# Optimization experiments

Hardware: AMD Instinct MI355X
Metric: run time of the kernel (lower is better)

The kernel has to match this reference:

```python
import jax, jax.numpy as jnp
import numpy as np

N, IN, H, D, OUT = 2048, 256, 12, 32, 384
ALPHA = 0.2


def setup_inputs() -> dict:
    key = jax.random.key(0)
    ks = jax.random.split(key, 12)
    s = 0.05
    return {
        "x": jax.random.normal(ks[0], (N, IN), jnp.float32),
        "adj": jax.random.uniform(ks[1], (N, N), jnp.float32),  # all > 0 -> fully connected mask
        "W": jax.random.normal(ks[2], (H * D, IN), jnp.float32) * s,
        "attn_src": jax.random.normal(ks[3], (H, D), jnp.float32) * s,
        "attn_dst": jax.random.normal(ks[4], (H, D), jnp.float32) * s,
        "edge_W": jax.random.normal(ks[5], (H, 1), jnp.float32) * s,
        "edge_b": jax.random.normal(ks[6], (H,), jnp.float32) * s,
        "res_W": jax.random.normal(ks[7], (H * D, IN), jnp.float32) * s,
        "res_b": jax.random.normal(ks[8], (H * D,), jnp.float32) * s,
        "fus_W": jax.random.normal(ks[9], (OUT, H * D), jnp.float32) * s,
        "fus_b": jax.random.normal(ks[10], (OUT,), jnp.float32) * s,
    }


def reference(x, adj, W, attn_src, attn_dst, edge_W, edge_b, res_W, res_b, fus_W, fus_b):
    n = x.shape[0]
    h = (x @ W.T).reshape(n, H, D)                      # [N,H,D]
    a_src = jnp.einsum("nhd,hd->nh", h, attn_src)       # [N,H]
    a_dst = jnp.einsum("nhd,hd->nh", h, attn_dst)       # [N,H]
    attn = a_src[:, None, :] + a_dst[None, :, :]        # [N,N,H]
    # edge_encoder: Linear(1 -> H) applied to adj[...,None]
    attn = attn + adj[..., None] * edge_W.reshape(1, 1, H) + edge_b
    mask = (adj > 0)[..., None]                         # [N,N,1]
    attn = jnp.where(mask, attn, -jnp.inf)
    attn = jnp.where(attn >= 0, attn, ALPHA * attn)     # leaky_relu
    attn = jax.nn.softmax(attn, axis=1)                 # over source nodes j
    # dropout is identity in eval mode
    h_out = jnp.einsum("ijh,jhd->ihd", attn, h).reshape(n, H * D)
    h_out = h_out + x @ res_W.T + res_b                 # residual
    out = jax.nn.gelu(h_out @ fus_W.T + fus_b, approximate=False)
    return out
```

## Files before the change

kernel.cpp:

```cpp
#include <hip/hip_runtime.h>
#include <hip/hip_bf16.h>

#define NN 2048
#define NH 12
#define HD 32
#define CALL 384

typedef float f32x16 __attribute__((ext_vector_type(16)));
typedef _Float16 f16x4 __attribute__((ext_vector_type(4)));
typedef __fp16 fp16x2 __attribute__((ext_vector_type(2)));

static __device__ __forceinline__ f32x16 mfma8f16(f16x4 a, f16x4 b, f32x16 c) {
    return __builtin_amdgcn_mfma_f32_32x32x8f16(a, b, c, 0, 0, 0);
}
static __device__ __forceinline__ f16x4 u2f(uint2 u) {
    union { uint2 u2; f16x4 f; } c; c.u2 = u; return c.f;
}
static __device__ __forceinline__ void gload16(const void* gp, void* lp) {
    __builtin_amdgcn_global_load_lds(
        (const __attribute__((address_space(1))) unsigned int*)gp,
        (__attribute__((address_space(3))) unsigned int*)lp, 16, 0, 0);
}

__global__ __launch_bounds__(512) void gemm01(
    const float* __restrict__ A, const float* __restrict__ B0,
    const float* __restrict__ B1, const float* __restrict__ bias1,
    const float* __restrict__ attn_src, const float* __restrict__ attn_dst,
    _Float16* __restrict__ outT, float* __restrict__ outF,
    float* __restrict__ asrc, float* __restrict__ adstT)
{
    __shared__ __align__(16) char smem[17408];
    _Float16 (*As)[68] = (_Float16(*)[68])(smem);
    _Float16 (*Bs)[68] = (_Float16(*)[68])(smem + 8704);
    float* red = (float*)smem;

    const int t = threadIdx.x;
    const int w = t >> 6, l = t & 63, g = l >> 5, il = l & 31;
    const int q = w & 3, kg = w >> 2;
    const int m0 = blockIdx.x * 64, n0 = blockIdx.y * 64;
    const int mode = blockIdx.z;
    const float* B = mode ? B1 : B0;
    const int wr = (q >> 1) * 32, wc = (q & 1) * 32;
    const int ti = t >> 3, seg = t & 7;
    const int Kdim = 256;

    const float* Abase = A + (size_t)(m0 + ti) * Kdim + seg * 8;
    const float* Bbase = B + (size_t)(n0 + ti) * Kdim + seg * 8;

    f32x16 acc;
#pragma unroll
    for (int r = 0; r < 16; ++r) acc[r] = 0.f;

    float4 av0 = *reinterpret_cast<const float4*>(Abase);
    float4 av1 = *reinterpret_cast<const float4*>(Abase + 4);
    float4 bv0 = *reinterpret_cast<const float4*>(Bbase);
    float4 bv1 = *reinterpret_cast<const float4*>(Bbase + 4);

#pragma unroll 1
    for (int ss = 0; ss < 4; ++ss) {
        __syncthreads();
        {
            f16x4 lo = {(_Float16)av0.x, (_Float16)av0.y, (_Float16)av0.z, (_Float16)av0.w};
            f16x4 hi = {(_Float16)av1.x, (_Float16)av1.y, (_Float16)av1.z, (_Float16)av1.w};
            *reinterpret_cast<f16x4*>(&As[ti][seg * 8])     = lo;
            *reinterpret_cast<f16x4*>(&As[ti][seg * 8 + 4]) = hi;
            f16x4 lo2 = {(_Float16)bv0.x, (_Float16)bv0.y, (_Float16)bv0.z, (_Float16)bv0.w};
            f16x4 hi2 = {(_Float16)bv1.x, (_Float16)bv1.y, (_Float16)bv1.z, (_Float16)bv1.w};
            *reinterpret_cast<f16x4*>(&Bs[ti][seg * 8])     = lo2;
            *reinterpret_cast<f16x4*>(&Bs[ti][seg * 8 + 4]) = hi2;
        }
        __syncthreads();
        if (ss < 3) {
            const int kk = (ss + 1) * 64;
            av0 = *reinterpret_cast<const float4*>(Abase + kk);
            av1 = *reinterpret_cast<const float4*>(Abase + kk + 4);
            bv0 = *reinterpret_cast<const float4*>(Bbase + kk);
            bv1 = *reinterpret_cast<const float4*>(Bbase + kk + 4);
        }
#pragma unroll
        for (int kc = 0; kc < 4; ++kc) {
            f16x4 af = *reinterpret_cast<const f16x4*>(&As[wr + il][kg * 32 + kc * 8 + 4 * g]);
            f16x4 bf = *reinterpret_cast<const f16x4*>(&Bs[wc + il][kg * 32 + kc * 8 + 4 * g]);
            acc = mfma8f16(af, bf, acc);
        }
    }

    __syncthreads();
    if (kg == 1) {
#pragma unroll
        for (int r = 0; r < 16; ++r) red[(q * 16 + r) * 64 + l] = acc[r];
    }
    __syncthreads();
    if (kg != 0) return;
#pragma unroll
    for (int r = 0; r < 16; ++r) acc[r] += red[(q * 16 + r) * 64 + l];

    const int colg = n0 + wc + il;
    if (mode == 0) {
#pragma unroll
        for (int p = 0; p < 4; ++p) {
            const int row = m0 + wr + 8 * p + 4 * g;
            f16x4 v;
#pragma unroll
            for (int r = 0; r < 4; ++r) v[r] = (_Float16)acc[4 * p + r];
            *reinterpret_cast<f16x4*>(&outT[(size_t)colg * NN + row]) = v;
        }
        const int hstar = colg >> 5;
        const float sv = attn_src[hstar * HD + il];
        const float dv = attn_dst[hstar * HD + il];
        float ps[16], pd[16];
#pragma unroll
        for (int r = 0; r < 16; ++r) { ps[r] = acc[r] * sv; pd[r] = acc[r] * dv; }
#pragma unroll
        for (int m = 1; m <= 16; m <<= 1) {
#pragma unroll
            for (int r = 0; r < 16; ++r) {
                ps[r] += __shfl_xor(ps[r], m);
                pd[r] += __shfl_xor(pd[r], m);
            }
        }
        if (il == 0) {
#pragma unroll
            for (int r = 0; r < 16; ++r) {
                const int row = m0 + wr + (r & 3) + 8 * (r >> 2) + 4 * g;
                asrc[row * NH + hstar] = ps[r];
                adstT[(size_t)hstar * NN + row] = pd[r] * 1.44269504089f;
            }
        }
    } else {
        const float bs = bias1[colg];
#pragma unroll
        for (int r = 0; r < 16; ++r) {
            const int row = m0 + wr + (r & 3) + 8 * (r >> 2) + 4 * g;
            outF[(size_t)row * CALL + colg] = acc[r] + bs;
        }
    }
}

__global__ __launch_bounds__(512) void gemm2(
    const _Float16* __restrict__ A16, const float* __restrict__ B,
    const float* __restrict__ bias, float* __restrict__ outF)
{
    __shared__ __align__(16) char smem[17408];
    _Float16 (*As)[68] = (_Float16(*)[68])(smem);
    _Float16 (*Bs)[68] = (_Float16(*)[68])(smem + 8704);
    float* red = (float*)smem;

    const int t = threadIdx.x;
    const int w = t >> 6, l = t & 63, g = l >> 5, il = l & 31;
    const int q = w & 3, kg = w >> 2;
    const int m0 = blockIdx.x * 64, n0 = blockIdx.y * 64;
    const int wr = (q >> 1) * 32, wc = (q & 1) * 32;
    const int ti = t >> 3, seg = t & 7;
    const int Kdim = 384;

    const _Float16* Abase = A16 + (size_t)(m0 + ti) * Kdim + seg * 8;
    const float*    Bbase = B   + (size_t)(n0 + ti) * Kdim + seg * 8;

    f32x16 acc;
#pragma unroll
    for (int r = 0; r < 16; ++r) acc[r] = 0.f;

    uint4  av = *reinterpret_cast<const uint4*>(Abase);
    float4 bv0 = *reinterpret_cast<const float4*>(Bbase);
    float4 bv1 = *reinterpret_cast<const float4*>(Bbase + 4);

#pragma unroll 1
    for (int ss = 0; ss < 6; ++ss) {
        __syncthreads();
        {
            *reinterpret_cast<uint2*>(&As[ti][seg * 8])     = make_uint2(av.x, av.y);
            *reinterpret_cast<uint2*>(&As[ti][seg * 8 + 4]) = make_uint2(av.z, av.w);
            f16x4 lo = {(_Float16)bv0.x, (_Float16)bv0.y, (_Float16)bv0.z, (_Float16)bv0.w};
            f16x4 hi = {(_Float16)bv1.x, (_Float16)bv1.y, (_Float16)bv1.z, (_Float16)bv1.w};
            *reinterpret_cast<f16x4*>(&Bs[ti][seg * 8])     = lo;
            *reinterpret_cast<f16x4*>(&Bs[ti][seg * 8 + 4]) = hi;
        }
        __syncthreads();
        if (ss < 5) {
            const int kk = (ss + 1) * 64;
            av  = *reinterpret_cast<const uint4*>(Abase + kk);
            bv0 = *reinterpret_cast<const float4*>(Bbase + kk);
            bv1 = *reinterpret_cast<const float4*>(Bbase + kk + 4);
        }
#pragma unroll
        for (int kc = 0; kc < 4; ++kc) {
            f16x4 af = *reinterpret_cast<const f16x4*>(&As[wr + il][kg * 32 + kc * 8 + 4 * g]);
            f16x4 bf = *reinterpret_cast<const f16x4*>(&Bs[wc + il][kg * 32 + kc * 8 + 4 * g]);
            acc = mfma8f16(af, bf, acc);
        }
    }

    __syncthreads();
    if (kg == 1) {
#pragma unroll
        for (int r = 0; r < 16; ++r) red[(q * 16 + r) * 64 + l] = acc[r];
    }
    __syncthreads();
    if (kg != 0) return;
#pragma unroll
    for (int r = 0; r < 16; ++r) acc[r] += red[(q * 16 + r) * 64 + l];

    const int colg = n0 + wc + il;
    const float bs = bias[colg];
#pragma unroll
    for (int r = 0; r < 16; ++r) {
        const int row = m0 + wr + (r & 3) + 8 * (r >> 2) + 4 * g;
        float vv = acc[r] + bs;
        vv = 0.5f * vv * (1.0f + erff(vv * 0.70710678118f));
        outF[(size_t)row * CALL + colg] = vv;
    }
}

__global__ __launch_bounds__(1024, 4) void attn17(
    const float* __restrict__ adj, const _Float16* __restrict__ hT,
    const float* __restrict__ asrc, const float* __restrict__ adstT,
    const float* __restrict__ eW, const float* __restrict__ eb,
    const float* __restrict__ res, _Float16* __restrict__ hsum)
{
    __shared__ __align__(16) char smem[90112];
    const int t = threadIdx.x;
    const int w = t >> 6, l = t & 63, g = l >> 5, il = l & 31;
    const int band = blockIdx.x & 63, hg = blockIdx.x >> 6;
    const int i0 = band * 32, h0 = hg * 3, c0 = hg * 96;

    char* slice   = smem + w * 5632;
    char* adjb    = slice;
    float* adst_s = (float*)(slice + 4096);
    float* red    = (float*)smem;
    float* dsum_s = (float*)(smem + 49152);

    const float LOG2E = 1.44269504089f;
    const int jbase = w * 128;
    const float* abase = adj + (size_t)(i0 + il) * NN + jbase + 16 * g;

#pragma unroll
    for (int p = 0; p < 4; ++p)
        gload16(abase + 4 * p, adjb + p * 1024);

    float base_h[3], eWr[3];
#pragma unroll
    for (int hh = 0; hh < 3; ++hh) {
        base_h[hh] = (asrc[(size_t)(i0 + il) * NH + h0 + hh] + eb[h0 + hh]) * LOG2E;
        eWr[hh] = eW[h0 + hh] * LOG2E;
    }
#pragma unroll
    for (int p = 0; p < 6; ++p) {
        const int idx = p * 64 + l;
        adst_s[idx] = adstT[(size_t)(h0 + (idx >> 7)) * NN + jbase + (idx & 127)];
    }

    f32x16 acc[3];
#pragma unroll
    for (int hh = 0; hh < 3; ++hh)
#pragma unroll
        for (int r = 0; r < 16; ++r) acc[hh][r] = 0.f;
    float4 dsumv[3];
#pragma unroll
    for (int hh = 0; hh < 3; ++hh) dsumv[hh] = make_float4(0.f, 0.f, 0.f, 0.f);

    const _Float16* hbase = hT + (size_t)(c0 + il) * NN + jbase + 16 * g;

#pragma unroll 1
    for (int tl = 0; tl < 4; ++tl) {
        const int jo = tl * 32;
        asm volatile("s_waitcnt vmcnt(0)" ::: "memory");
        const float4 aj0 = *reinterpret_cast<const float4*>(adjb + 0 * 1024 + l * 16);
        const float4 aj1 = *reinterpret_cast<const float4*>(adjb + 1 * 1024 + l * 16);
        const float4 aj2 = *reinterpret_cast<const float4*>(adjb + 2 * 1024 + l * 16);
        const float4 aj3 = *reinterpret_cast<const float4*>(adjb + 3 * 1024 + l * 16);
        asm volatile("s_waitcnt lgkmcnt(0)" ::: "memory");
        if (tl < 3) {
#pragma unroll
            for (int p = 0; p < 4; ++p)
                gload16(abase + jo + 32 + 4 * p, adjb + p * 1024);
        }
        __builtin_amdgcn_s_setprio(1);
#pragma unroll
        for (int hh = 0; hh < 3; ++hh) {
            const _Float16* hp = hbase + (size_t)(hh * 32) * NN + jo;
            const uint4 hA = *reinterpret_cast<const uint4*>(hp);
            const uint4 hB = *reinterpret_cast<const uint4*>(hp + 8);
#pragma unroll
            for (int ks = 0; ks < 4; ++ks) {
                const float4 a4 = (ks == 0) ? aj0 : (ks == 1) ? aj1 : (ks == 2) ? aj2 : aj3;
                const float4 ad = *reinterpret_cast<const float4*>(
                    &adst_s[hh * 128 + jo + 16 * g + 4 * ks]);
                float e0, e1, e2, e3;
#pragma unroll
                for (int jj = 0; jj < 4; ++jj) {
                    const float ajv = (&a4.x)[jj];
                    float tt = fmaf(ajv, eWr[hh], base_h[hh] + (&ad.x)[jj]);
                    tt = fmaxf(tt, 0.2f * tt);
                    const float ee = ajv > 0.f ? __builtin_amdgcn_exp2f(tt) : 0.f;
                    (&dsumv[hh].x)[jj] += ee;
                    (jj == 0 ? e0 : jj == 1 ? e1 : jj == 2 ? e2 : e3) = ee;
                }
                union { fp16x2 h2[2]; f16x4 h4; } u;
                u.h2[0] = __builtin_amdgcn_cvt_pkrtz(e0, e1);
                u.h2[1] = __builtin_amdgcn_cvt_pkrtz(e2, e3);
                const uint2 hu = (ks == 0) ? make_uint2(hA.x, hA.y)
                               : (ks == 1) ? make_uint2(hA.z, hA.w)
                               : (ks == 2) ? make_uint2(hB.x, hB.y)
                                           : make_uint2(hB.z, hB.w);
                acc[hh] = mfma8f16(u.h4, u2f(hu), acc[hh]);
            }
        }
        __builtin_amdgcn_s_setprio(0);
    }

    __syncthreads();
#pragma unroll
    for (int hh = 0; hh < 3; ++hh) {
        const float ds = (dsumv[hh].x + dsumv[hh].y) + (dsumv[hh].z + dsumv[hh].w);
        const float dtot = ds + __shfl_xor(ds, 32);
        if (g == 0) dsum_s[(w * 3 + hh) * 32 + il] = dtot;
    }
    if (w < 4) {
#pragma unroll
        for (int hh = 0; hh < 3; ++hh)
#pragma unroll
            for (int reg = 0; reg < 16; ++reg)
                red[((w * 3 + hh) * 16 + reg) * 64 + l] = acc[hh][reg];
    }
    __syncthreads();
    if (w >= 4 && w < 8) {
#pragma unroll
        for (int hh = 0; hh < 3; ++hh)
#pragma unroll
            for (int reg = 0; reg < 16; ++reg)
                red[(((w - 4) * 3 + hh) * 16 + reg) * 64 + l] += acc[hh][reg];
    }
    __syncthreads();
    if (w >= 8 && w < 12) {
#pragma unroll
        for (int hh = 0; hh < 3; ++hh)
#pragma unroll
            for (int reg = 0; reg < 16; ++reg)
                red[(((w - 8) * 3 + hh) * 16 + reg) * 64 + l] += acc[hh][reg];
    }
    __syncthreads();
    if (w >= 12) {
#pragma unroll
        for (int hh = 0; hh < 3; ++hh)
#pragma unroll
            for (int reg = 0; reg < 16; ++reg)
                red[(((w - 12) * 3 + hh) * 16 + reg) * 64 + l] += acc[hh][reg];
    }
    __syncthreads();

    {
        const int reg = w;
        const int row_off = (reg & 3) + 8 * (reg >> 2) + 4 * g;
        const int row = i0 + row_off;
#pragma unroll
        for (int hh = 0; hh < 3; ++hh) {
            float v = 0.f, d = 0.f;
#pragma unroll
            for (int p = 0; p < 4; ++p)
                v += red[((p * 3 + hh) * 16 + reg) * 64 + l];
#pragma unroll
            for (int ww = 0; ww < 16; ++ww)
                d += dsum_s[(ww * 3 + hh) * 32 + row_off];
            const float inv = __builtin_amdgcn_rcpf(d);
            const int col = (h0 + hh) * 32 + il;
            hsum[(size_t)row * CALL + col] = (_Float16)(v * inv + res[(size_t)row * CALL + col]);
        }
    }
}

extern "C" void kernel_launch(void* const* d_in, const int* in_sizes, int n_in,
                              void* d_out, int out_size, void* d_ws, size_t ws_size,
                              hipStream_t stream)
{
    const float* x        = (const float*)d_in[0];
    const float* adj      = (const float*)d_in[1];
    const float* W        = (const float*)d_in[2];
    const float* attn_src = (const float*)d_in[3];
    const float* attn_dst = (const float*)d_in[4];
    const float* edge_W   = (const float*)d_in[5];
    const float* edge_b   = (const float*)d_in[6];
    const float* res_W    = (const float*)d_in[7];
    const float* res_b    = (const float*)d_in[8];
    const float* fus_W    = (const float*)d_in[9];
    const float* fus_b    = (const float*)d_in[10];
    float* out = (float*)d_out;

    char* ws = (char*)d_ws;
    size_t off = 0;
    auto alloc = [&](size_t bytes) { void* p = ws + off; off = (off + bytes + 255) & ~(size_t)255; return p; };
    _Float16* hT    = (_Float16*)alloc((size_t)CALL * NN * 2);
    float*    res   = (float*)alloc((size_t)NN * CALL * 4);
    float*    asrc  = (float*)alloc((size_t)NN * NH * 4);
    float*    adstT = (float*)alloc((size_t)NH * NN * 4);
    _Float16* hsum  = (_Float16*)alloc((size_t)NN * CALL * 2);
    (void)ws_size;

    gemm01<<<dim3(32, 6, 2), dim3(512), 0, stream>>>(x, W, res_W, res_b, attn_src, attn_dst, hT, res, asrc, adstT);
    attn17<<<256, dim3(1024), 0, stream>>>(adj, hT, asrc, adstT, edge_W, edge_b, res, hsum);
    gemm2<<<dim3(32, 6), dim3(512), 0, stream>>>(hsum, fus_W, fus_b, out);
}
```

Before: 49.47 us.

## Split attention kernel per head with XCD-aware block mapping and smaller blocks

The attention kernel now has each block handle one head instead of three, with 512 threads, 256 source columns per wave and 768 blocks instead of 256. Blocks are mapped so that each XCD shares the same row bands, which aims at L2 reuse of adj rows, and sched barriers pin the load ordering. This cuts per-block LDS and registers for higher occupancy and a shorter cross-wave reduction. In exchange, each adj tile is now re-read and re-exponentiated-loaded once per head rather than once per three heads.

Result: slower. 58.98 us (+19.2%).

```diff
diff --git a/kernel.cpp b/kernel.cpp
--- a/kernel.cpp
+++ b/kernel.cpp
@@ -212,57 +212,50 @@
     }
 }
 
-__global__ __launch_bounds__(1024, 4) void attn17(
+__global__ __launch_bounds__(512, 6) void attn18(
     const float* __restrict__ adj, const _Float16* __restrict__ hT,
     const float* __restrict__ asrc, const float* __restrict__ adstT,
     const float* __restrict__ eW, const float* __restrict__ eb,
     const float* __restrict__ res, _Float16* __restrict__ hsum)
 {
-    __shared__ __align__(16) char smem[90112];
+    __shared__ __align__(16) char smem[40960];
     const int t = threadIdx.x;
     const int w = t >> 6, l = t & 63, g = l >> 5, il = l & 31;
-    const int band = blockIdx.x & 63, hg = blockIdx.x >> 6;
-    const int i0 = band * 32, h0 = hg * 3, c0 = hg * 96;
-
-    char* slice   = smem + w * 5632;
+    const int b = blockIdx.x;
+    const int xcd = b & 7, qq = b >> 3;
+    const int h = qq % NH, bw = qq / NH;
+    const int band = xcd * 8 + bw;
+    const int i0 = band * 32, c0 = h * 32;
+
+    char* slice   = smem + w * 5120;
     char* adjb    = slice;
     float* adst_s = (float*)(slice + 4096);
     float* red    = (float*)smem;
-    float* dsum_s = (float*)(smem + 49152);
+    float* dsum_s = (float*)(smem + 16384);
 
     const float LOG2E = 1.44269504089f;
-    const int jbase = w * 128;
+    const int jbase = w * 256;
     const float* abase = adj + (size_t)(i0 + il) * NN + jbase + 16 * g;
 
 #pragma unroll
     for (int p = 0; p < 4; ++p)
         gload16(abase + 4 * p, adjb + p * 1024);
 
-    float base_h[3], eWr[3];
-#pragma unroll
-    for (int hh = 0; hh < 3; ++hh) {
-        base_h[hh] = (asrc[(size_t)(i0 + il) * NH + h0 + hh] + eb[h0 + hh]) * LOG2E;
-        eWr[hh] = eW[h0 + hh] * LOG2E;
-    }
-#pragma unroll
-    for (int p = 0; p < 6; ++p) {
-        const int idx = p * 64 + l;
-        adst_s[idx] = adstT[(size_t)(h0 + (idx >> 7)) * NN + jbase + (idx & 127)];
-    }
-
-    f32x16 acc[3];
-#pragma unroll
-    for (int hh = 0; hh < 3; ++hh)
-#pragma unroll
-        for (int r = 0; r < 16; ++r) acc[hh][r] = 0.f;
-    float4 dsumv[3];
-#pragma unroll
-    for (int hh = 0; hh < 3; ++hh) dsumv[hh] = make_float4(0.f, 0.f, 0.f, 0.f);
+    const float base = (asrc[(size_t)(i0 + il) * NH + h] + eb[h]) * LOG2E;
+    const float eWr  = eW[h] * LOG2E;
+#pragma unroll
+    for (int p = 0; p < 4; ++p)
+        adst_s[p * 64 + l] = adstT[(size_t)h * NN + jbase + p * 64 + l];
+
+    f32x16 acc;
+#pragma unroll
+    for (int r = 0; r < 16; ++r) acc[r] = 0.f;
+    float4 dsumv = make_float4(0.f, 0.f, 0.f, 0.f);
 
     const _Float16* hbase = hT + (size_t)(c0 + il) * NN + jbase + 16 * g;
 
 #pragma unroll 1
-    for (int tl = 0; tl < 4; ++tl) {
+    for (int tl = 0; tl < 8; ++tl) {
         const int jo = tl * 32;
         asm volatile("s_waitcnt vmcnt(0)" ::: "memory");
         const float4 aj0 = *reinterpret_cast<const float4*>(adjb + 0 * 1024 + l * 16);
@@ -270,102 +263,75 @@
         const float4 aj2 = *reinterpret_cast<const float4*>(adjb + 2 * 1024 + l * 16);
         const float4 aj3 = *reinterpret_cast<const float4*>(adjb + 3 * 1024 + l * 16);
         asm volatile("s_waitcnt lgkmcnt(0)" ::: "memory");
-        if (tl < 3) {
+        __builtin_amdgcn_sched_barrier(0);
+        const _Float16* hp = hbase + jo;
+        const uint4 hA = *reinterpret_cast<const uint4*>(hp);
+        const uint4 hB = *reinterpret_cast<const uint4*>(hp + 8);
+        __builtin_amdgcn_sched_barrier(0);
+        if (tl < 7) {
 #pragma unroll
             for (int p = 0; p < 4; ++p)
                 gload16(abase + jo + 32 + 4 * p, adjb + p * 1024);
         }
-        __builtin_amdgcn_s_setprio(1);
-#pragma unroll
-        for (int hh = 0; hh < 3; ++hh) {
-            const _Float16* hp = hbase + (size_t)(hh * 32) * NN + jo;
-            const uint4 hA = *reinterpret_cast<const uint4*>(hp);
-            const uint4 hB = *reinterpret_cast<const uint4*>(hp + 8);
-#pragma unroll
-            for (int ks = 0; ks < 4; ++ks) {
-                const float4 a4 = (ks == 0) ? aj0 : (ks == 1) ? aj1 : (ks == 2) ? aj2 : aj3;
-                const float4 ad = *reinterpret_cast<const float4*>(
-                    &adst_s[hh * 128 + jo + 16 * g + 4 * ks]);
-                float e0, e1, e2, e3;
-#pragma unroll
-                for (int jj = 0; jj < 4; ++jj) {
-                    const float ajv = (&a4.x)[jj];
-                    float tt = fmaf(ajv, eWr[hh], base_h[hh] + (&ad.x)[jj]);
-                    tt = fmaxf(tt, 0.2f * tt);
-                    const float ee = ajv > 0.f ? __builtin_amdgcn_exp2f(tt) : 0.f;
-                    (&dsumv[hh].x)[jj] += ee;
-                    (jj == 0 ? e0 : jj == 1 ? e1 : jj == 2 ? e2 : e3) = ee;
-                }
-                union { fp16x2 h2[2]; f16x4 h4; } u;
-                u.h2[0] = __builtin_amdgcn_cvt_pkrtz(e0, e1);
-                u.h2[1] = __builtin_amdgcn_cvt_pkrtz(e2, e3);
-                const uint2 hu = (ks == 0) ? make_uint2(hA.x, hA.y)
-                               : (ks == 1) ? make_uint2(hA.z, hA.w)
-                               : (ks == 2) ? make_uint2(hB.x, hB.y)
-                                           : make_uint2(hB.z, hB.w);
-                acc[hh] = mfma8f16(u.h4, u2f(hu), acc[hh]);
+        __builtin_amdgcn_sched_barrier(0);
+#pragma unroll
+        for (int ks = 0; ks < 4; ++ks) {
+            const float4 a4 = (ks == 0) ? aj0 : (ks == 1) ? aj1 : (ks == 2) ? aj2 : aj3;
+            const float4 ad = *reinterpret_cast<const float4*>(
+                &adst_s[jo + 16 * g + 4 * ks]);
+            float e0, e1, e2, e3;
+#pragma unroll
+            for (int jj = 0; jj < 4; ++jj) {
+                const float ajv = (&a4.x)[jj];
+                float tt = fmaf(ajv, eWr, base + (&ad.x)[jj]);
+                tt = fmaxf(tt, 0.2f * tt);
+                const float ee = ajv > 0.f ? __builtin_amdgcn_exp2f(tt) : 0.f;
+                (&dsumv.x)[jj] += ee;
+                (jj == 0 ? e0 : jj == 1 ? e1 : jj == 2 ? e2 : e3) = ee;
             }
-        }
-        __builtin_amdgcn_s_setprio(0);
-    }
-
-    __syncthreads();
-#pragma unroll
-    for (int hh = 0; hh < 3; ++hh) {
-        const float ds = (dsumv[hh].x + dsumv[hh].y) + (dsumv[hh].z + dsumv[hh].w);
-        const float dtot = ds + __shfl_xor(ds, 32);
-        if (g == 0) dsum_s[(w * 3 + hh) * 32 + il] = dtot;
+            union { fp16x2 h2[2]; f16x4 h4; } u;
+            u.h2[0] = __builtin_amdgcn_cvt_pkrtz(e0, e1);
+            u.h2[1] = __builtin_amdgcn_cvt_pkrtz(e2, e3);
+            const uint2 hu = (ks == 0) ? make_uint2(hA.x, hA.y)
+                           : (ks == 1) ? make_uint2(hA.z, hA.w)
+                           : (ks == 2) ? make_uint2(hB.x, hB.y)
+                                       : make_uint2(hB.z, hB.w);
+            acc = mfma8f16(u.h4, u2f(hu), acc);
+        }
+    }
+
+    __syncthreads();
+    {
+        float dt = (dsumv.x + dsumv.y) + (dsumv.z + dsumv.w);
+        dt += __shfl_xor(dt, 32);
+        if (g == 0) dsum_s[w * 32 + il] = dt;
     }
     if (w < 4) {
 #pragma unroll
-        for (int hh = 0; hh < 3; ++hh)
-#pragma unroll
-            for (int reg = 0; reg < 16; ++reg)
-                red[((w * 3 + hh) * 16 + reg) * 64 + l] = acc[hh][reg];
-    }
-    __syncthreads();
-    if (w >= 4 && w < 8) {
-#pragma unroll
-        for (int hh = 0; hh < 3; ++hh)
-#pragma unroll
-            for (int reg = 0; reg < 16; ++reg)
-                red[(((w - 4) * 3 + hh) * 16 + reg) * 64 + l] += acc[hh][reg];
-    }
-    __syncthreads();
-    if (w >= 8 && w < 12) {
-#pragma unroll
-        for (int hh = 0; hh < 3; ++hh)
-#pragma unroll
-            for (int reg = 0; reg < 16; ++reg)
-                red[(((w - 8) * 3 + hh) * 16 + reg) * 64 + l] += acc[hh][reg];
-    }
-    __syncthreads();
-    if (w >= 12) {
-#pragma unroll
-        for (int hh = 0; hh < 3; ++hh)
-#pragma unroll
-            for (int reg = 0; reg < 16; ++reg)
-                red[(((w - 12) * 3 + hh) * 16 + reg) * 64 + l] += acc[hh][reg];
-    }
-    __syncthreads();
-
-    {
-        const int reg = w;
+        for (int r = 0; r < 16; ++r) red[(w * 16 + r) * 64 + l] = acc[r];
+    }
+    __syncthreads();
+    if (w >= 4) {
+#pragma unroll
+        for (int r = 0; r < 16; ++r) red[((w - 4) * 16 + r) * 64 + l] += acc[r];
+    }
+    __syncthreads();
+
+#pragma unroll
+    for (int rr = 0; rr < 2; ++rr) {
+        const int reg = w + rr * 8;
         const int row_off = (reg & 3) + 8 * (reg >> 2) + 4 * g;
         const int row = i0 + row_off;
-#pragma unroll
-        for (int hh = 0; hh < 3; ++hh) {
-            float v = 0.f, d = 0.f;
-#pragma unroll
-            for (int p = 0; p < 4; ++p)
-                v += red[((p * 3 + hh) * 16 + reg) * 64 + l];
-#pragma unroll
-            for (int ww = 0; ww < 16; ++ww)
-                d += dsum_s[(ww * 3 + hh) * 32 + row_off];
-            const float inv = __builtin_amdgcn_rcpf(d);
-            const int col = (h0 + hh) * 32 + il;
-            hsum[(size_t)row * CALL + col] = (_Float16)(v * inv + res[(size_t)row * CALL + col]);
-        }
+        float v = 0.f, d = 0.f;
+#pragma unroll
+        for (int p = 0; p < 4; ++p)
+            v += red[(p * 16 + reg) * 64 + l];
+#pragma unroll
+        for (int ww = 0; ww < 8; ++ww)
+            d += dsum_s[ww * 32 + row_off];
+        const float inv = __builtin_amdgcn_rcpf(d);
+        const int col = c0 + il;
+        hsum[(size_t)row * CALL + col] = (_Float16)(v * inv + res[(size_t)row * CALL + col]);
     }
 }
 
@@ -397,6 +363,6 @@
     (void)ws_size;
 
     gemm01<<<dim3(32, 6, 2), dim3(512), 0, stream>>>(x, W, res_W, res_b, attn_src, attn_dst, hT, res, asrc, adstT);
-    attn17<<<256, dim3(1024), 0, stream>>>(adj, hT, asrc, adstT, edge_W, edge_b, res, hsum);
+    attn18<<<768, dim3(512), 0, stream>>>(adj, hT, asrc, adstT, edge_W, edge_b, res, hsum);
     gemm2<<<dim3(32, 6), dim3(512), 0, stream>>>(hsum, fus_W, fus_b, out);
 }
```

## Store h in MFMA fragment-native layout and prefetch fragments before adj reload

Applied to the files above, without the earlier changes.

The projection GEMM now writes h in a layout that matches the MFMA B-operand fragments of the attention kernel, indexed by j-tile, head and k-step. Each lane in the attention kernel then reads one contiguous 8-byte fragment per k-step, so consecutive lanes hit consecutive addresses instead of strided rows of a transposed matrix. The fragment loads for all three heads are issued up front behind scheduling barriers, before the next adj prefetch, to overlap their latency with compute. The cost is scattered 2-byte stores in the GEMM epilogue, which replace the vectorized 4-wide stores, plus more registers held live in the attention loop.

Result: faster. 46.25 us (median of 2 runs) (-6.5%).

```diff
diff --git a/kernel.cpp b/kernel.cpp
--- a/kernel.cpp
+++ b/kernel.cpp
@@ -22,11 +22,12 @@
         (__attribute__((address_space(3))) unsigned int*)lp, 16, 0, 0);
 }
 
+
 __global__ __launch_bounds__(512) void gemm01(
     const float* __restrict__ A, const float* __restrict__ B0,
     const float* __restrict__ B1, const float* __restrict__ bias1,
     const float* __restrict__ attn_src, const float* __restrict__ attn_dst,
-    _Float16* __restrict__ outT, float* __restrict__ outF,
+    _Float16* __restrict__ hF, float* __restrict__ outF,
     float* __restrict__ asrc, float* __restrict__ adstT)
 {
     __shared__ __align__(16) char smem[17408];
@@ -97,15 +98,16 @@
 
     const int colg = n0 + wc + il;
     if (mode == 0) {
-#pragma unroll
-        for (int p = 0; p < 4; ++p) {
-            const int row = m0 + wr + 8 * p + 4 * g;
-            f16x4 v;
-#pragma unroll
-            for (int r = 0; r < 4; ++r) v[r] = (_Float16)acc[4 * p + r];
-            *reinterpret_cast<f16x4*>(&outT[(size_t)colg * NN + row]) = v;
-        }
         const int hstar = colg >> 5;
+#pragma unroll
+        for (int r = 0; r < 16; ++r) {
+            const int j = m0 + wr + (r & 3) + 8 * (r >> 2) + 4 * g;
+            const int jt = j >> 5, jin = j & 31;
+            const int g_f = jin >> 4, ks_f = (jin & 15) >> 2, e = jin & 3;
+            const int lane_f = 32 * g_f + il;
+            hF[(size_t)(((jt * NH + hstar) * 4 + ks_f) * 256) + lane_f * 4 + e] =
+                (_Float16)acc[r];
+        }
         const float sv = attn_src[hstar * HD + il];
         const float dv = attn_dst[hstar * HD + il];
         float ps[16], pd[16];
@@ -212,8 +214,8 @@
     }
 }
 
-__global__ __launch_bounds__(1024, 4) void attn17(
-    const float* __restrict__ adj, const _Float16* __restrict__ hT,
+__global__ __launch_bounds__(1024, 4) void attn19(
+    const float* __restrict__ adj, const _Float16* __restrict__ hF,
     const float* __restrict__ asrc, const float* __restrict__ adstT,
     const float* __restrict__ eW, const float* __restrict__ eb,
     const float* __restrict__ res, _Float16* __restrict__ hsum)
@@ -222,7 +224,7 @@
     const int t = threadIdx.x;
     const int w = t >> 6, l = t & 63, g = l >> 5, il = l & 31;
     const int band = blockIdx.x & 63, hg = blockIdx.x >> 6;
-    const int i0 = band * 32, h0 = hg * 3, c0 = hg * 96;
+    const int i0 = band * 32, h0 = hg * 3;
 
     char* slice   = smem + w * 5632;
     char* adjb    = slice;
@@ -259,28 +261,35 @@
 #pragma unroll
     for (int hh = 0; hh < 3; ++hh) dsumv[hh] = make_float4(0.f, 0.f, 0.f, 0.f);
 
-    const _Float16* hbase = hT + (size_t)(c0 + il) * NN + jbase + 16 * g;
-
 #pragma unroll 1
     for (int tl = 0; tl < 4; ++tl) {
         const int jo = tl * 32;
+        const int jt = w * 4 + tl;
         asm volatile("s_waitcnt vmcnt(0)" ::: "memory");
         const float4 aj0 = *reinterpret_cast<const float4*>(adjb + 0 * 1024 + l * 16);
         const float4 aj1 = *reinterpret_cast<const float4*>(adjb + 1 * 1024 + l * 16);
         const float4 aj2 = *reinterpret_cast<const float4*>(adjb + 2 * 1024 + l * 16);
         const float4 aj3 = *reinterpret_cast<const float4*>(adjb + 3 * 1024 + l * 16);
         asm volatile("s_waitcnt lgkmcnt(0)" ::: "memory");
+        __builtin_amdgcn_sched_barrier(0);
+        uint2 hf[3][4];
+#pragma unroll
+        for (int hh = 0; hh < 3; ++hh) {
+            const _Float16* fp = hF + (size_t)(((jt * NH + h0 + hh) * 4) * 256) + l * 4;
+#pragma unroll
+            for (int ks = 0; ks < 4; ++ks)
+                hf[hh][ks] = *reinterpret_cast<const uint2*>(fp + ks * 256);
+        }
+        __builtin_amdgcn_sched_barrier(0);
         if (tl < 3) {
 #pragma unroll
             for (int p = 0; p < 4; ++p)
                 gload16(abase + jo + 32 + 4 * p, adjb + p * 1024);
         }
+        __builtin_amdgcn_sched_barrier(0);
         __builtin_amdgcn_s_setprio(1);
 #pragma unroll
         for (int hh = 0; hh < 3; ++hh) {
-            const _Float16* hp = hbase + (size_t)(hh * 32) * NN + jo;
-            const uint4 hA = *reinterpret_cast<const uint4*>(hp);
-            const uint4 hB = *reinterpret_cast<const uint4*>(hp + 8);
 #pragma unroll
             for (int ks = 0; ks < 4; ++ks) {
                 const float4 a4 = (ks == 0) ? aj0 : (ks == 1) ? aj1 : (ks == 2) ? aj2 : aj3;
@@ -299,11 +308,7 @@
                 union { fp16x2 h2[2]; f16x4 h4; } u;
                 u.h2[0] = __builtin_amdgcn_cvt_pkrtz(e0, e1);
                 u.h2[1] = __builtin_amdgcn_cvt_pkrtz(e2, e3);
-                const uint2 hu = (ks == 0) ? make_uint2(hA.x, hA.y)
-                               : (ks == 1) ? make_uint2(hA.z, hA.w)
-                               : (ks == 2) ? make_uint2(hB.x, hB.y)
-                                           : make_uint2(hB.z, hB.w);
-                acc[hh] = mfma8f16(u.h4, u2f(hu), acc[hh]);
+                acc[hh] = mfma8f16(u.h4, u2f(hf[hh][ks]), acc[hh]);
             }
         }
         __builtin_amdgcn_s_setprio(0);
@@ -389,14 +394,14 @@
     char* ws = (char*)d_ws;
     size_t off = 0;
     auto alloc = [&](size_t bytes) { void* p = ws + off; off = (off + bytes + 255) & ~(size_t)255; return p; };
-    _Float16* hT    = (_Float16*)alloc((size_t)CALL * NN * 2);
+    _Float16* hF    = (_Float16*)alloc((size_t)64 * NH * 4 * 256 * 2);
     float*    res   = (float*)alloc((size_t)NN * CALL * 4);
     float*    asrc  = (float*)alloc((size_t)NN * NH * 4);
     float*    adstT = (float*)alloc((size_t)NH * NN * 4);
     _Float16* hsum  = (_Float16*)alloc((size_t)NN * CALL * 2);
     (void)ws_size;
 
-    gemm01<<<dim3(32, 6, 2), dim3(512), 0, stream>>>(x, W, res_W, res_b, attn_src, attn_dst, hT, res, asrc, adstT);
-    attn17<<<256, dim3(1024), 0, stream>>>(adj, hT, asrc, adstT, edge_W, edge_b, res, hsum);
+    gemm01<<<dim3(32, 6, 2), dim3(512), 0, stream>>>(x, W, res_W, res_b, attn_src, attn_dst, hF, res, asrc, adstT);
+    attn19<<<256, dim3(1024), 0, stream>>>(adj, hF, asrc, adstT, edge_W, edge_b, res, hsum);
     gemm2<<<dim3(32, 6), dim3(512), 0, stream>>>(hsum, fus_W, fus_b, out);
 }
```
